# Kernel optimization log

Measured on AMD Instinct MI355X. Metric: run time of the kernel, lower is better.

The kernel has to match this reference:

```python
import jax, jax.numpy as jnp
import numpy as np


def setup_inputs() -> dict:
    key = jax.random.key(0)
    k1, k2, k3, k4 = jax.random.split(key, 4)
    B, L, V, F, D = 32, 4096, 10, 1024, 64
    indices = jax.random.randint(k1, (B, L), 0, V, dtype=jnp.int64)
    fp_table = jax.random.normal(k2, (V, F), dtype=jnp.float32)
    W = jax.random.normal(k3, (D, F), dtype=jnp.float32) * 0.03
    b = jax.random.normal(k4, (D,), dtype=jnp.float32) * 0.01
    return {"indices": indices, "fp_table": fp_table, "W": W, "b": b}


def reference(indices, fp_table, W, b):
    # Per-character fingerprint lookup: [B, L, F]
    emb = fp_table[indices]
    # Linear 1024 -> dim: [B, L, D]
    proj = jnp.einsum('blf,df->bld', emb, W) + b
    # Original: per-sequence [L, D] -> transpose -> [D, L]; vstack over batch -> [B*D, L];
    # reshape(-1, B*D, L) -> [1, B*D, L]
    B, L, D = proj.shape
    out = jnp.transpose(proj, (0, 2, 1)).reshape(B * D, L)
    return out.reshape(1, B * D, L)
```

## Files before the change

### kernel.cpp

```cpp
#include <hip/hip_runtime.h>

#define B_SIZE 32
#define L_SIZE 4096
#define V_SIZE 10
#define F_SIZE 1024
#define D_SIZE 64

__global__ __launch_bounds__(64) void fp_proj_kernel(
    const float* __restrict__ fp_table,
    const float* __restrict__ W,
    const float* __restrict__ bias,
    float* __restrict__ Pt) {
  const int o = blockIdx.x;
  const int v = o / D_SIZE;
  const int d = o % D_SIZE;
  const int lane = threadIdx.x;

  const float4* ft4 = (const float4*)(fp_table + v * F_SIZE);
  const float4* w4  = (const float4*)(W + d * F_SIZE);

  float sum = 0.f;
  for (int i = lane; i < F_SIZE / 4; i += 64) {
    float4 a = ft4[i];
    float4 b = w4[i];
    sum += a.x * b.x + a.y * b.y + a.z * b.z + a.w * b.w;
  }
  #pragma unroll
  for (int off = 32; off > 0; off >>= 1)
    sum += __shfl_down(sum, off, 64);

  if (lane == 0) Pt[d * V_SIZE + v] = sum + bias[d];
}

__global__ __launch_bounds__(256) void gather_kernel(
    const int* __restrict__ idx,
    const float* __restrict__ Pt,
    float* __restrict__ out) {
  __shared__ float Pl[D_SIZE * V_SIZE];
  for (int i = threadIdx.x; i < D_SIZE * V_SIZE; i += 256) Pl[i] = Pt[i];
  __syncthreads();

  const int g  = blockIdx.x * 256 + threadIdx.x;
  const int r  = g >> 10;
  const int c4 = g & 1023;
  const int b  = r >> 6;
  const int d  = r & 63;

  const int4 vi = ((const int4*)idx)[b * (L_SIZE / 4) + c4];

  const float* Pd = Pl + d * V_SIZE;
  float4 o;
  o.x = Pd[vi.x];
  o.y = Pd[vi.y];
  o.z = Pd[vi.z];
  o.w = Pd[vi.w];

  ((float4*)out)[g] = o;
}

extern "C" void kernel_launch(void* const* d_in, const int* in_sizes, int n_in,
                              void* d_out, int out_size, void* d_ws, size_t ws_size,
                              hipStream_t stream) {
  const int*   idx      = (const int*)d_in[0];
  const float* fp_table = (const float*)d_in[1];
  const float* W        = (const float*)d_in[2];
  const float* bias     = (const float*)d_in[3];
  float* out = (float*)d_out;
  float* Pt  = (float*)d_ws;

  fp_proj_kernel<<<V_SIZE * D_SIZE, 64, 0, stream>>>(fp_table, W, bias, Pt);

  const int total4 = B_SIZE * D_SIZE * (L_SIZE / 4);
  gather_kernel<<<total4 / 256, 256, 0, stream>>>(idx, Pt, out);
}
```

Before: 75.61 us.

## Fuse projection table computation into gather kernel, recomputing per output row

Replaces the two-kernel scheme (project the 10-entry fingerprint table, then gather) with one kernel that has a block per (batch, d) row. Ten wavefronts each compute one dot product for that row's column of the projected table into shared memory, then all 1024 threads gather and write the row. This removes one kernel launch and the workspace round trip. In exchange the projection is recomputed 32 times per d (once per batch), and each block does 40KB of fp_table/W reads before its 16KB of output, which raises L2 traffic and delays the stores.

```diff
diff --git a/kernel.cpp b/kernel.cpp
--- a/kernel.cpp
+++ b/kernel.cpp
@@ -5,57 +5,48 @@
 #define V_SIZE 10
 #define F_SIZE 1024
 #define D_SIZE 64
+#define L4     (L_SIZE / 4)
 
-__global__ __launch_bounds__(64) void fp_proj_kernel(
+__global__ __launch_bounds__(1024) void fused_fp_embed(
+    const int* __restrict__ idx,
     const float* __restrict__ fp_table,
     const float* __restrict__ W,
     const float* __restrict__ bias,
-    float* __restrict__ Pt) {
-  const int o = blockIdx.x;
-  const int v = o / D_SIZE;
-  const int d = o % D_SIZE;
-  const int lane = threadIdx.x;
+    float* __restrict__ out) {
+  const int r    = blockIdx.x;
+  const int b    = r >> 6;
+  const int d    = r & 63;
+  const int t    = threadIdx.x;
+  const int wv   = t >> 6;
+  const int lane = t & 63;
 
-  const float4* ft4 = (const float4*)(fp_table + v * F_SIZE);
-  const float4* w4  = (const float4*)(W + d * F_SIZE);
+  __shared__ float Pd[16];
 
-  float sum = 0.f;
-  for (int i = lane; i < F_SIZE / 4; i += 64) {
-    float4 a = ft4[i];
-    float4 b = w4[i];
-    sum += a.x * b.x + a.y * b.y + a.z * b.z + a.w * b.w;
+  const int4 vi = ((const int4*)idx)[b * L4 + t];
+
+  if (wv < V_SIZE) {
+    const float4* ft4 = (const float4*)(fp_table + wv * F_SIZE);
+    const float4* w4  = (const float4*)(W + d * F_SIZE);
+    float sum = 0.f;
+    #pragma unroll
+    for (int i = 0; i < 4; ++i) {
+      float4 a = ft4[lane + 64 * i];
+      float4 w = w4[lane + 64 * i];
+      sum += a.x * w.x + a.y * w.y + a.z * w.z + a.w * w.w;
+    }
+    #pragma unroll
+    for (int off = 32; off > 0; off >>= 1)
+      sum += __shfl_down(sum, off, 64);
+    if (lane == 0) Pd[wv] = sum + bias[d];
   }
-  #pragma unroll
-  for (int off = 32; off > 0; off >>= 1)
-    sum += __shfl_down(sum, off, 64);
-
-  if (lane == 0) Pt[d * V_SIZE + v] = sum + bias[d];
-}
-
-__global__ __launch_bounds__(256) void gather_kernel(
-    const int* __restrict__ idx,
-    const float* __restrict__ Pt,
-    float* __restrict__ out) {
-  __shared__ float Pl[D_SIZE * V_SIZE];
-  for (int i = threadIdx.x; i < D_SIZE * V_SIZE; i += 256) Pl[i] = Pt[i];
   __syncthreads();
 
-  const int g  = blockIdx.x * 256 + threadIdx.x;
-  const int r  = g >> 10;
-  const int c4 = g & 1023;
-  const int b  = r >> 6;
-  const int d  = r & 63;
-
-  const int4 vi = ((const int4*)idx)[b * (L_SIZE / 4) + c4];
-
-  const float* Pd = Pl + d * V_SIZE;
   float4 o;
   o.x = Pd[vi.x];
   o.y = Pd[vi.y];
   o.z = Pd[vi.z];
   o.w = Pd[vi.w];
-
-  ((float4*)out)[g] = o;
+  ((float4*)out)[r * L4 + t] = o;
 }
 
 extern "C" void kernel_launch(void* const* d_in, const int* in_sizes, int n_in,
@@ -66,10 +57,7 @@
   const float* W        = (const float*)d_in[2];
   const float* bias     = (const float*)d_in[3];
   float* out = (float*)d_out;
-  float* Pt  = (float*)d_ws;
+  (void)d_ws; (void)ws_size;
 
-  fp_proj_kernel<<<V_SIZE * D_SIZE, 64, 0, stream>>>(fp_table, W, bias, Pt);
-
-  const int total4 = B_SIZE * D_SIZE * (L_SIZE / 4);
-  gather_kernel<<<total4 / 256, 256, 0, stream>>>(idx, Pt, out);
+  fused_fp_embed<<<B_SIZE * D_SIZE, 1024, 0, stream>>>(idx, fp_table, W, bias, out);
 }
```

New measurement: 75.98 us. No clear change (+0.5%).
